# Optimization experiments

Measured on AMD Instinct MI355X. Metric: run time of the kernel, lower is better.

The kernel has to match this reference:

```python
import jax, jax.numpy as jnp
import numpy as np

B, S, D, H = 2, 2048, 1024, 16
DK = D // H


def setup_inputs() -> dict:
    key = jax.random.key(0)
    ks = jax.random.split(key, 12)
    scale = 1.0 / np.sqrt(D)
    inp = {
        "query": jax.random.normal(ks[0], (B, S, D), jnp.float32),
        "key": jax.random.normal(ks[1], (B, S, D), jnp.float32),
        "value": jax.random.normal(ks[2], (B, S, D), jnp.float32),
        # causal mask [B, S, S]; 0 -> masked
        "mask": jnp.broadcast_to(jnp.tril(jnp.ones((S, S), jnp.int32)), (B, S, S)),
        "Wq": jax.random.normal(ks[3], (D, D), jnp.float32) * scale,
        "bq": jnp.zeros((D,), jnp.float32),
        "Wk": jax.random.normal(ks[4], (D, D), jnp.float32) * scale,
        "bk": jnp.zeros((D,), jnp.float32),
        "Wv": jax.random.normal(ks[5], (D, D), jnp.float32) * scale,
        "bv": jnp.zeros((D,), jnp.float32),
        "Wo": jax.random.normal(ks[6], (D, D), jnp.float32) * scale,
        "bo": jnp.zeros((D,), jnp.float32),
    }
    return inp


def reference(query, key, value, mask, Wq, bq, Wk, bk, Wv, bv, Wo, bo):
    # linear projections (torch Linear: x @ W^T + b)
    q = query @ Wq.T + bq
    k = key @ Wk.T + bk
    v = value @ Wv.T + bv
    # [B, S, D] -> [B, H, S, DK]
    def split_heads(x):
        return x.reshape(B, -1, H, DK).transpose(0, 2, 1, 3)
    q, k, v = split_heads(q), split_heads(k), split_heads(v)
    scores = jnp.einsum("bhqd,bhkd->bhqk", q, k) / jnp.sqrt(jnp.float32(DK))
    # mask unsqueezed at dim 1 -> broadcast over heads; 0 entries get -inf
    scores = jnp.where(mask[:, None, :, :] == 0, -jnp.inf, scores)
    p_attn = jax.nn.softmax(scores, axis=-1)  # dropout p=0 (eval)
    x = jnp.einsum("bhqk,bhkd->bhqd", p_attn, v)
    x = x.transpose(0, 2, 1, 3).reshape(B, -1, D)
    return x @ Wo.T + bo
```

## Files before the change

kernel.cpp:

```cpp
#include <hip/hip_runtime.h>
#include <hip/hip_bf16.h>

#define Bb 2
#define Ss 2048
#define Dd 1024
#define Hh 16
#define DKk 64
#define Mm (Bb*Ss)

typedef __bf16 bf16;
typedef __attribute__((ext_vector_type(8))) __bf16 bf16x8;
typedef __attribute__((ext_vector_type(4))) __bf16 bf16x4;
typedef __attribute__((ext_vector_type(4))) float  f32x4;

#define MFMA(Af, Bf, Cf) __builtin_amdgcn_mfma_f32_16x16x32_bf16(Af, Bf, Cf, 0, 0, 0)

__device__ __forceinline__ void gld_lds16(const void* g, void* l) {
  __builtin_amdgcn_global_load_lds(
      (const __attribute__((address_space(1))) void*)g,
      (__attribute__((address_space(3))) void*)l, 16, 0, 0);
}

__global__ __launch_bounds__(256) void cvt_f32_bf16(
    const float* __restrict__ s, bf16* __restrict__ d, int n4) {
  int i = blockIdx.x * 256 + threadIdx.x;
  if (i >= n4) return;
  float4 v = reinterpret_cast<const float4*>(s)[i];
  bf16x4 o;
  o[0] = (bf16)v.x; o[1] = (bf16)v.y; o[2] = (bf16)v.z; o[3] = (bf16)v.w;
  reinterpret_cast<bf16x4*>(d)[i] = o;
}

template <bool F32OUT>
__global__ __launch_bounds__(256) void gemm_bt(
    const bf16* __restrict__ A, const bf16* __restrict__ W,
    const float* __restrict__ bias, bf16* __restrict__ out_bf,
    float* __restrict__ out_f32) {
  constexpr int N = 1024, K = 1024;
  __shared__ bf16 As[128 * 32];
  __shared__ bf16 Bs[128 * 32];
  const int tid = threadIdx.x;
  const int w = tid >> 6, lane = tid & 63;
  const int wr = w >> 1, wc = w & 1;
  const int row0 = blockIdx.y * 128, col0 = blockIdx.x * 128;
  const bf16* Ab = A + (size_t)row0 * K;
  const bf16* Wb = W + (size_t)col0 * K;

  f32x4 acc[4][4] = {};

  for (int kt = 0; kt < K / 32; ++kt) {
    const int k0 = kt * 32;
#pragma unroll
    for (int i = 0; i < 2; ++i) {
      const int c = i * 4 + w;
      const int r = c * 16 + (lane >> 2);
      const int ce = (lane & 3) * 8;
      gld_lds16(Ab + (size_t)r * K + k0 + ce, (char*)As + c * 1024);
      gld_lds16(Wb + (size_t)r * K + k0 + ce, (char*)Bs + c * 1024);
    }
    __syncthreads();

    bf16x8 af[4], bfr[4];
#pragma unroll
    for (int m = 0; m < 4; ++m) {
      const int r = wr * 64 + m * 16 + (lane & 15);
      af[m] = *(const bf16x8*)&As[r * 32 + (lane >> 4) * 8];
    }
#pragma unroll
    for (int n = 0; n < 4; ++n) {
      const int r = wc * 64 + n * 16 + (lane & 15);
      bfr[n] = *(const bf16x8*)&Bs[r * 32 + (lane >> 4) * 8];
    }
#pragma unroll
    for (int m = 0; m < 4; ++m)
#pragma unroll
      for (int n = 0; n < 4; ++n)
        acc[m][n] = MFMA(af[m], bfr[n], acc[m][n]);
    __syncthreads();
  }

  const int g = lane >> 4, c15 = lane & 15;
#pragma unroll
  for (int n = 0; n < 4; ++n) {
    const int col = col0 + wc * 64 + n * 16 + c15;
    const float bv = bias[col];
#pragma unroll
    for (int m = 0; m < 4; ++m) {
      const int rbase = row0 + wr * 64 + m * 16 + g * 4;
#pragma unroll
      for (int r = 0; r < 4; ++r) {
        const float v = acc[m][n][r] + bv;
        if (F32OUT) out_f32[(size_t)(rbase + r) * N + col] = v;
        else        out_bf [(size_t)(rbase + r) * N + col] = (bf16)v;
      }
    }
  }
}

__global__ __launch_bounds__(256) void attn_fwd(
    const bf16* __restrict__ Q, const bf16* __restrict__ K,
    const bf16* __restrict__ V, bf16* __restrict__ X) {
  __shared__ bf16 Ks[2][64][32];
  __shared__ bf16 Vs[2][64][32];
  __shared__ bf16 Ps[4][16][64];

  const int tid = threadIdx.x;
  const int w = tid >> 6, lane = tid & 63;
  const int z = blockIdx.x & 15, bh = blockIdx.x >> 4;
  const int b = bh >> 4, h = bh & 15;

  const bf16* Qb = Q + (size_t)b * Ss * Dd + h * DKk;
  const bf16* Kb = K + (size_t)b * Ss * Dd + h * DKk;
  const bf16* Vb = V + (size_t)b * Ss * Dd + h * DKk;
  bf16* Xb = X + (size_t)b * Ss * Dd + h * DKk;

  for (int pass = 0; pass < 2; ++pass) {
    const int qt = pass ? z : 31 - z;
    const int q0 = qt * 64;

    bf16x8 qf[2];
    {
      const int qr = q0 + w * 16 + (lane & 15);
      const int d0 = (lane >> 4) * 8;
      qf[0] = *(const bf16x8*)&Qb[(size_t)qr * Dd + d0];
      qf[1] = *(const bf16x8*)&Qb[(size_t)qr * Dd + d0 + 32];
    }

    f32x4 of[4] = {};
    float m_run[4], l_run[4];
#pragma unroll
    for (int r = 0; r < 4; ++r) { m_run[r] = -INFINITY; l_run[r] = 0.f; }

    const int nchunks = qt + 1;
    for (int ct = 0; ct < nchunks; ++ct) {
      const int kv0 = ct * 64;
#pragma unroll
      for (int i = 0; i < 2; ++i) {
        const int c = i * 4 + w;
        const int ks = c >> 2;
        const int kvl = (c & 3) * 16 + (lane >> 2);
        const int dl = (lane & 3) * 8;
        gld_lds16(Kb + (size_t)(kv0 + kvl) * Dd + ks * 32 + dl,
                  (char*)Ks + c * 1024);
      }
      {
        const int p = tid >> 3;
        const int d0 = (tid & 7) * 8;
        const int kv = 2 * p;
        const int kh = kv >> 5, kvlo = kv & 31;
        bf16x8 v0 = *(const bf16x8*)&Vb[(size_t)(kv0 + kv) * Dd + d0];
        bf16x8 v1 = *(const bf16x8*)&Vb[(size_t)(kv0 + kv + 1) * Dd + d0];
#pragma unroll
        for (int j = 0; j < 8; ++j) {
          bf16* dst = &Vs[kh][d0 + j][kvlo];
          dst[0] = v0[j];
          dst[1] = v1[j];
        }
      }
      __syncthreads();

      f32x4 sf[4] = {};
#pragma unroll
      for (int n = 0; n < 4; ++n) {
#pragma unroll
        for (int ks = 0; ks < 2; ++ks) {
          bf16x8 kf = *(const bf16x8*)&Ks[ks][n * 16 + (lane & 15)][(lane >> 4) * 8];
          sf[n] = MFMA(qf[ks], kf, sf[n]);
        }
      }

      const int qrb = q0 + w * 16 + (lane >> 4) * 4;
      float mchunk[4];
#pragma unroll
      for (int r = 0; r < 4; ++r) mchunk[r] = -INFINITY;
#pragma unroll
      for (int n = 0; n < 4; ++n) {
        const int kvcol = kv0 + n * 16 + (lane & 15);
#pragma unroll
        for (int r = 0; r < 4; ++r) {
          float sv = sf[n][r] * 0.125f;
          if (kvcol > qrb + r) sv = -INFINITY;
          sf[n][r] = sv;
          mchunk[r] = fmaxf(mchunk[r], sv);
        }
      }
#pragma unroll
      for (int off = 1; off < 16; off <<= 1)
#pragma unroll
        for (int r = 0; r < 4; ++r)
          mchunk[r] = fmaxf(mchunk[r], __shfl_xor(mchunk[r], off, 64));

      float alpha[4], rsum[4];
#pragma unroll
      for (int r = 0; r < 4; ++r) {
        const float mn = fmaxf(m_run[r], mchunk[r]);
        alpha[r] = __expf(m_run[r] - mn);
        m_run[r] = mn;
        rsum[r] = 0.f;
      }
#pragma unroll
      for (int n = 0; n < 4; ++n)
#pragma unroll
        for (int r = 0; r < 4; ++r) {
          const float p = __expf(sf[n][r] - m_run[r]);
          rsum[r] += p;
          Ps[w][(lane >> 4) * 4 + r][n * 16 + (lane & 15)] = (bf16)p;
        }
#pragma unroll
      for (int off = 1; off < 16; off <<= 1)
#pragma unroll
        for (int r = 0; r < 4; ++r)
          rsum[r] += __shfl_xor(rsum[r], off, 64);
#pragma unroll
      for (int r = 0; r < 4; ++r)
        l_run[r] = l_run[r] * alpha[r] + rsum[r];
#pragma unroll
      for (int n = 0; n < 4; ++n)
#pragma unroll
        for (int r = 0; r < 4; ++r)
          of[n][r] *= alpha[r];

#pragma unroll
      for (int ks = 0; ks < 2; ++ks) {
        bf16x8 pfr = *(const bf16x8*)&Ps[w][lane & 15][ks * 32 + (lane >> 4) * 8];
#pragma unroll
        for (int n = 0; n < 4; ++n) {
          bf16x8 vf = *(const bf16x8*)&Vs[ks][n * 16 + (lane & 15)][(lane >> 4) * 8];
          of[n] = MFMA(pfr, vf, of[n]);
        }
      }
      __syncthreads();
    }

#pragma unroll
    for (int n = 0; n < 4; ++n)
#pragma unroll
      for (int r = 0; r < 4; ++r) {
        const int q = q0 + w * 16 + (lane >> 4) * 4 + r;
        const float v = of[n][r] / l_run[r];
        Xb[(size_t)q * Dd + n * 16 + (lane & 15)] = (bf16)v;
      }
  }
}

extern "C" void kernel_launch(void* const* d_in, const int* in_sizes, int n_in,
                              void* d_out, int out_size, void* d_ws, size_t ws_size,
                              hipStream_t stream) {
  const float* query = (const float*)d_in[0];
  const float* key   = (const float*)d_in[1];
  const float* value = (const float*)d_in[2];
  const float* Wq = (const float*)d_in[4];
  const float* bq = (const float*)d_in[5];
  const float* Wk = (const float*)d_in[6];
  const float* bk = (const float*)d_in[7];
  const float* Wv = (const float*)d_in[8];
  const float* bv = (const float*)d_in[9];
  const float* Wo = (const float*)d_in[10];
  const float* bo = (const float*)d_in[11];

  char* ws = (char*)d_ws;
  bf16* qb  = (bf16*)(ws + (0ull  << 20));
  bf16* kb  = (bf16*)(ws + (8ull  << 20));
  bf16* vb  = (bf16*)(ws + (16ull << 20));
  bf16* wqb = (bf16*)(ws + (24ull << 20));
  bf16* wkb = (bf16*)(ws + (26ull << 20));
  bf16* wvb = (bf16*)(ws + (28ull << 20));
  bf16* wob = (bf16*)(ws + (30ull << 20));
  bf16* Qp  = (bf16*)(ws + (32ull << 20));
  bf16* Kp  = (bf16*)(ws + (40ull << 20));
  bf16* Vp  = (bf16*)(ws + (48ull << 20));
  bf16* Xa  = (bf16*)(ws + (56ull << 20));

  const int NT4 = (Bb * Ss * Dd) / 4;
  const int NW4 = (Dd * Dd) / 4;

  cvt_f32_bf16<<<NT4 / 256, 256, 0, stream>>>(query, qb, NT4);
  cvt_f32_bf16<<<NT4 / 256, 256, 0, stream>>>(key,   kb, NT4);
  cvt_f32_bf16<<<NT4 / 256, 256, 0, stream>>>(value, vb, NT4);
  cvt_f32_bf16<<<NW4 / 256, 256, 0, stream>>>(Wq, wqb, NW4);
  cvt_f32_bf16<<<NW4 / 256, 256, 0, stream>>>(Wk, wkb, NW4);
  cvt_f32_bf16<<<NW4 / 256, 256, 0, stream>>>(Wv, wvb, NW4);
  cvt_f32_bf16<<<NW4 / 256, 256, 0, stream>>>(Wo, wob, NW4);

  dim3 gg(8, 32);
  gemm_bt<false><<<gg, 256, 0, stream>>>(qb, wqb, bq, Qp, nullptr);
  gemm_bt<false><<<gg, 256, 0, stream>>>(kb, wkb, bk, Kp, nullptr);
  gemm_bt<false><<<gg, 256, 0, stream>>>(vb, wvb, bv, Vp, nullptr);

  attn_fwd<<<512, 256, 0, stream>>>(Qp, Kp, Vp, Xa);

  gemm_bt<true><<<gg, 256, 0, stream>>>(Xa, wob, bo, nullptr, (float*)d_out);
}
```

Measured before the change: 334.1 us.

## Merge conversion kernels and batch QKV projections into single launches

The seven separate fp32-to-bf16 conversion launches become one prep kernel that selects its source by block index. The three QKV projection GEMMs become one launch over a 24x32 grid that picks input, bias and output per 1024-column section, which fills the device better. The output projection now uses 64-row tiles with four column-split waves, doubling its block count to 512 to raise occupancy. The cost is a more generic GEMM template with branching in the tile-load loop.

```diff
diff --git a/kernel.cpp b/kernel.cpp
--- a/kernel.cpp
+++ b/kernel.cpp
@@ -6,7 +6,6 @@
 #define Dd 1024
 #define Hh 16
 #define DKk 64
-#define Mm (Bb*Ss)
 
 typedef __bf16 bf16;
 typedef __attribute__((ext_vector_type(8))) __bf16 bf16x8;
@@ -21,68 +20,98 @@
       (__attribute__((address_space(3))) void*)l, 16, 0, 0);
 }
 
-__global__ __launch_bounds__(256) void cvt_f32_bf16(
-    const float* __restrict__ s, bf16* __restrict__ d, int n4) {
-  int i = blockIdx.x * 256 + threadIdx.x;
-  if (i >= n4) return;
-  float4 v = reinterpret_cast<const float4*>(s)[i];
+__global__ __launch_bounds__(256) void prep(
+    const float* __restrict__ q, const float* __restrict__ k, const float* __restrict__ v,
+    const float* __restrict__ Wq, const float* __restrict__ Wk, const float* __restrict__ Wv,
+    const float* __restrict__ Wo,
+    bf16* __restrict__ qb, bf16* __restrict__ kb, bf16* __restrict__ vb,
+    bf16* __restrict__ wqkv, bf16* __restrict__ wob) {
+  const int bid = blockIdx.x;
+  const float* src; bf16* dst; int idx;
+  if (bid < 4096)       { src = q;  dst = qb; idx = bid; }
+  else if (bid < 8192)  { src = k;  dst = kb; idx = bid - 4096; }
+  else if (bid < 12288) { src = v;  dst = vb; idx = bid - 8192; }
+  else if (bid < 13312) { src = Wq; dst = wqkv;              idx = bid - 12288; }
+  else if (bid < 14336) { src = Wk; dst = wqkv + (1u << 20); idx = bid - 13312; }
+  else if (bid < 15360) { src = Wv; dst = wqkv + (2u << 20); idx = bid - 14336; }
+  else                  { src = Wo; dst = wob;               idx = bid - 15360; }
+  const int i = idx * 256 + threadIdx.x;
+  float4 x = reinterpret_cast<const float4*>(src)[i];
   bf16x4 o;
-  o[0] = (bf16)v.x; o[1] = (bf16)v.y; o[2] = (bf16)v.z; o[3] = (bf16)v.w;
-  reinterpret_cast<bf16x4*>(d)[i] = o;
-}
-
-template <bool F32OUT>
+  o[0] = (bf16)x.x; o[1] = (bf16)x.y; o[2] = (bf16)x.z; o[3] = (bf16)x.w;
+  reinterpret_cast<bf16x4*>(dst)[i] = o;
+}
+
+template <int BM, int WC, bool QKV, bool F32OUT>
 __global__ __launch_bounds__(256) void gemm_bt(
-    const bf16* __restrict__ A, const bf16* __restrict__ W,
-    const float* __restrict__ bias, bf16* __restrict__ out_bf,
-    float* __restrict__ out_f32) {
-  constexpr int N = 1024, K = 1024;
-  __shared__ bf16 As[128 * 32];
+    const bf16* __restrict__ A0, const bf16* __restrict__ A1, const bf16* __restrict__ A2,
+    const bf16* __restrict__ W,
+    const float* __restrict__ b0, const float* __restrict__ b1, const float* __restrict__ b2,
+    bf16* __restrict__ o0, bf16* __restrict__ o1, bf16* __restrict__ o2,
+    float* __restrict__ of32) {
+  constexpr int K = 1024;
+  constexpr int NFR = 128 / (16 * WC);
+  constexpr int ACH = BM / 16;
+  constexpr int NCH = (ACH + 8) / 4;
+  __shared__ bf16 As[BM * 32];
   __shared__ bf16 Bs[128 * 32];
+
   const int tid = threadIdx.x;
   const int w = tid >> 6, lane = tid & 63;
-  const int wr = w >> 1, wc = w & 1;
-  const int row0 = blockIdx.y * 128, col0 = blockIdx.x * 128;
+  const int wr = (WC == 2) ? (w >> 1) : 0;
+  const int wc = (WC == 2) ? (w & 1) : w;
+  const int row0 = blockIdx.y * BM, col0 = blockIdx.x * 128;
+
+  const int sec = QKV ? (col0 >> 10) : 0;
+  const bf16* A    = QKV ? (sec == 0 ? A0 : sec == 1 ? A1 : A2) : A0;
+  const float* bias= QKV ? (sec == 0 ? b0 : sec == 1 ? b1 : b2) : b0;
+  bf16* outb       = QKV ? (sec == 0 ? o0 : sec == 1 ? o1 : o2) : o0;
+  const int cols0  = col0 & 1023;
   const bf16* Ab = A + (size_t)row0 * K;
   const bf16* Wb = W + (size_t)col0 * K;
 
-  f32x4 acc[4][4] = {};
+  f32x4 acc[4][NFR] = {};
 
   for (int kt = 0; kt < K / 32; ++kt) {
     const int k0 = kt * 32;
 #pragma unroll
-    for (int i = 0; i < 2; ++i) {
-      const int c = i * 4 + w;
-      const int r = c * 16 + (lane >> 2);
+    for (int i = 0; i < NCH; ++i) {
+      const int cc = i * 4 + w;
+      const int rl = lane >> 2;
       const int ce = (lane & 3) * 8;
-      gld_lds16(Ab + (size_t)r * K + k0 + ce, (char*)As + c * 1024);
-      gld_lds16(Wb + (size_t)r * K + k0 + ce, (char*)Bs + c * 1024);
+      if (cc < ACH) {
+        const int r = cc * 16 + rl;
+        gld_lds16(Ab + (size_t)r * K + k0 + ce, (char*)As + cc * 1024);
+      } else {
+        const int r = (cc - ACH) * 16 + rl;
+        gld_lds16(Wb + (size_t)r * K + k0 + ce, (char*)Bs + (cc - ACH) * 1024);
+      }
     }
     __syncthreads();
 
-    bf16x8 af[4], bfr[4];
+    bf16x8 af[4], bfr[NFR];
 #pragma unroll
     for (int m = 0; m < 4; ++m) {
       const int r = wr * 64 + m * 16 + (lane & 15);
       af[m] = *(const bf16x8*)&As[r * 32 + (lane >> 4) * 8];
     }
 #pragma unroll
-    for (int n = 0; n < 4; ++n) {
-      const int r = wc * 64 + n * 16 + (lane & 15);
+    for (int n = 0; n < NFR; ++n) {
+      const int r = wc * (16 * NFR) + n * 16 + (lane & 15);
       bfr[n] = *(const bf16x8*)&Bs[r * 32 + (lane >> 4) * 8];
     }
 #pragma unroll
     for (int m = 0; m < 4; ++m)
 #pragma unroll
-      for (int n = 0; n < 4; ++n)
+      for (int n = 0; n < NFR; ++n)
         acc[m][n] = MFMA(af[m], bfr[n], acc[m][n]);
     __syncthreads();
   }
 
   const int g = lane >> 4, c15 = lane & 15;
 #pragma unroll
-  for (int n = 0; n < 4; ++n) {
-    const int col = col0 + wc * 64 + n * 16 + c15;
+  for (int n = 0; n < NFR; ++n) {
+    const int col = cols0 + wc * (16 * NFR) + n * 16 + c15;
     const float bv = bias[col];
 #pragma unroll
     for (int m = 0; m < 4; ++m) {
@@ -90,8 +119,8 @@
 #pragma unroll
       for (int r = 0; r < 4; ++r) {
         const float v = acc[m][n][r] + bv;
-        if (F32OUT) out_f32[(size_t)(rbase + r) * N + col] = v;
-        else        out_bf [(size_t)(rbase + r) * N + col] = (bf16)v;
+        if (F32OUT) of32[(size_t)(rbase + r) * 1024 + col] = v;
+        else        outb[(size_t)(rbase + r) * 1024 + col] = (bf16)v;
       }
     }
   }
@@ -259,35 +288,25 @@
   const float* bo = (const float*)d_in[11];
 
   char* ws = (char*)d_ws;
-  bf16* qb  = (bf16*)(ws + (0ull  << 20));
-  bf16* kb  = (bf16*)(ws + (8ull  << 20));
-  bf16* vb  = (bf16*)(ws + (16ull << 20));
-  bf16* wqb = (bf16*)(ws + (24ull << 20));
-  bf16* wkb = (bf16*)(ws + (26ull << 20));
-  bf16* wvb = (bf16*)(ws + (28ull << 20));
-  bf16* wob = (bf16*)(ws + (30ull << 20));
-  bf16* Qp  = (bf16*)(ws + (32ull << 20));
-  bf16* Kp  = (bf16*)(ws + (40ull << 20));
-  bf16* Vp  = (bf16*)(ws + (48ull << 20));
-  bf16* Xa  = (bf16*)(ws + (56ull << 20));
-
-  const int NT4 = (Bb * Ss * Dd) / 4;
-  const int NW4 = (Dd * Dd) / 4;
-
-  cvt_f32_bf16<<<NT4 / 256, 256, 0, stream>>>(query, qb, NT4);
-  cvt_f32_bf16<<<NT4 / 256, 256, 0, stream>>>(key,   kb, NT4);
-  cvt_f32_bf16<<<NT4 / 256, 256, 0, stream>>>(value, vb, NT4);
-  cvt_f32_bf16<<<NW4 / 256, 256, 0, stream>>>(Wq, wqb, NW4);
-  cvt_f32_bf16<<<NW4 / 256, 256, 0, stream>>>(Wk, wkb, NW4);
-  cvt_f32_bf16<<<NW4 / 256, 256, 0, stream>>>(Wv, wvb, NW4);
-  cvt_f32_bf16<<<NW4 / 256, 256, 0, stream>>>(Wo, wob, NW4);
-
-  dim3 gg(8, 32);
-  gemm_bt<false><<<gg, 256, 0, stream>>>(qb, wqb, bq, Qp, nullptr);
-  gemm_bt<false><<<gg, 256, 0, stream>>>(kb, wkb, bk, Kp, nullptr);
-  gemm_bt<false><<<gg, 256, 0, stream>>>(vb, wvb, bv, Vp, nullptr);
+  bf16* qb   = (bf16*)(ws + (0ull  << 20));
+  bf16* kb   = (bf16*)(ws + (8ull  << 20));
+  bf16* vb   = (bf16*)(ws + (16ull << 20));
+  bf16* wqkv = (bf16*)(ws + (24ull << 20));
+  bf16* wob  = (bf16*)(ws + (30ull << 20));
+  bf16* Qp   = (bf16*)(ws + (32ull << 20));
+  bf16* Kp   = (bf16*)(ws + (40ull << 20));
+  bf16* Vp   = (bf16*)(ws + (48ull << 20));
+  bf16* Xa   = (bf16*)(ws + (56ull << 20));
+
+  prep<<<16384, 256, 0, stream>>>(query, key, value, Wq, Wk, Wv, Wo,
+                                  qb, kb, vb, wqkv, wob);
+
+  gemm_bt<128, 2, true, false><<<dim3(24, 32), 256, 0, stream>>>(
+      qb, kb, vb, wqkv, bq, bk, bv, Qp, Kp, Vp, nullptr);
 
   attn_fwd<<<512, 256, 0, stream>>>(Qp, Kp, Vp, Xa);
 
-  gemm_bt<true><<<gg, 256, 0, stream>>>(Xa, wob, bo, nullptr, (float*)d_out);
-}
+  gemm_bt<64, 4, false, true><<<dim3(8, 64), 256, 0, stream>>>(
+      Xa, nullptr, nullptr, wob, bo, nullptr, nullptr,
+      nullptr, nullptr, nullptr, (float*)d_out);
+}
```

New measurement: 291.6 us. 12.7% less time.
